# Performance work log

Measured on AMD Instinct MI355X. Metric: run time of the kernel, lower is better.

The kernel has to match this reference:

```python
import jax, jax.numpy as jnp
import numpy as np

K = 5  # filter_size (matches init_kwargs)


def _adaptive_pool_matrix(size: int, k: int) -> jnp.ndarray:
    """Row-stochastic [k, size] matrix replicating torch adaptive_avg_pool1d bins."""
    P = np.zeros((k, size), np.float32)
    for i in range(k):
        s = (i * size) // k
        e = -((-(i + 1) * size) // k)  # ceil((i+1)*size/k)
        P[i, s:e] = 1.0 / (e - s)
    return jnp.asarray(P)


def setup_inputs() -> dict:
    key = jax.random.key(0)
    k1, k2, k3 = jax.random.split(key, 3)
    B, Cin, Cout, H, W = 8, 32, 32, 256, 256
    x = jax.random.normal(k1, (B, Cin, H, W), jnp.float32)
    conv_w = jax.random.normal(k2, (Cout, Cin), jnp.float32) * (1.0 / np.sqrt(Cin))
    conv_b = jax.random.normal(k3, (Cout,), jnp.float32) * 0.01
    return {"x": x, "conv_w": conv_w, "conv_b": conv_b}


def reference(x, conv_w, conv_b):
    B, Cin, H, W = x.shape
    # 1x1 conv == channel-mixing einsum
    feat = jnp.einsum('bihw,oi->bohw', x, conv_w) + conv_b[None, :, None, None]
    C = feat.shape[1]
    # adaptive_avg_pool2d(feat, K) via static pooling matrices -> per-(b,c) KxK filter
    Ph = _adaptive_pool_matrix(H, K)
    Pw = _adaptive_pool_matrix(W, K)
    filt = jnp.einsum('kh,bchw,lw->bckl', Ph, feat, Pw)  # [B, C, K, K]
    # pad per original intent ('same' output), then grouped conv with groups=B*C
    pad = (K - 1) // 2
    if (K - 1) % 2 == 0:
        p = ((pad, pad), (pad, pad))
    else:
        p = ((pad + 1, pad), (pad + 1, pad))
    inp = feat.reshape(1, B * C, H, W)
    w = filt.reshape(B * C, 1, K, K)
    out = jax.lax.conv_general_dilated(
        inp, w, window_strides=(1, 1), padding=p,
        dimension_numbers=('NCHW', 'OIHW', 'NCHW'),
        feature_group_count=B * C)
    return out.reshape(B, C, H, W)
```

## Files before the change

kernel.cpp:

```cpp
#include <hip/hip_runtime.h>


#define CIN 32
#define COUT 32
#define HW 256
#define PLANE (HW * HW)
#define BATCH 8
#define KF 5
#define BIN 52

__global__ __launch_bounds__(256) void conv1x1_kernel(const float* __restrict__ x,
                                                      const float* __restrict__ Wm,
                                                      const float* __restrict__ bias,
                                                      float* __restrict__ feat) {
    int b  = blockIdx.x >> 6;
    int rg = blockIdx.x & 63;
    int p0 = rg * 1024 + threadIdx.x * 4;

    const float* xb = x + (size_t)b * CIN * PLANE + p0;
    float4 xv[CIN];
#pragma unroll
    for (int i = 0; i < CIN; ++i) xv[i] = *(const float4*)(xb + (size_t)i * PLANE);

    float* fb = feat + (size_t)b * COUT * PLANE + p0;
#pragma unroll 4
    for (int o = 0; o < COUT; ++o) {
        float bv = bias[o];
        float4 a; a.x = bv; a.y = bv; a.z = bv; a.w = bv;
#pragma unroll
        for (int i = 0; i < CIN; ++i) {
            float wv = Wm[o * CIN + i];
            a.x += wv * xv[i].x; a.y += wv * xv[i].y;
            a.z += wv * xv[i].z; a.w += wv * xv[i].w;
        }
        *(float4*)(fb + (size_t)o * PLANE) = a;
    }
}

__global__ __launch_bounds__(256) void pool_kernel(const float* __restrict__ feat,
                                                   float* __restrict__ filt) {
    int bo = blockIdx.x / KF;
    int k  = blockIdx.x % KF;
    int sk = (k * HW) / KF;
    int t  = threadIdx.x;
    int c4 = t & 63;
    int rq = t >> 6;

    const float* f = feat + (size_t)bo * PLANE + (sk + rq) * HW + c4 * 4;
    float4 a = {0.f, 0.f, 0.f, 0.f};
#pragma unroll
    for (int j = 0; j < 13; ++j) {
        float4 v = *(const float4*)(f + j * 4 * HW);
        a.x += v.x; a.y += v.y; a.z += v.z; a.w += v.w;
    }

    __shared__ float4 red[256];
    __shared__ float cols[256];
    red[t] = a;
    __syncthreads();
    if (t < 64) {
        float4 r0 = red[t], r1 = red[t + 64], r2 = red[t + 128], r3 = red[t + 192];
        cols[4 * t + 0] = r0.x + r1.x + r2.x + r3.x;
        cols[4 * t + 1] = r0.y + r1.y + r2.y + r3.y;
        cols[4 * t + 2] = r0.z + r1.z + r2.z + r3.z;
        cols[4 * t + 3] = r0.w + r1.w + r2.w + r3.w;
    }
    __syncthreads();
    if (t < KF) {
        int sl = (t * HW) / KF;
        float s = 0.f;
        for (int w = 0; w < BIN; ++w) s += cols[sl + w];
        filt[bo * 25 + k * KF + t] = s * (1.0f / (BIN * BIN));
    }
}

#define LROW 264
__global__ __launch_bounds__(256) void dwconv_kernel(const float* __restrict__ feat,
                                                     const float* __restrict__ filt,
                                                     float* __restrict__ out) {
    int bo    = blockIdx.y;
    int strip = blockIdx.x;
    int gy0   = strip * 32;
    int t     = threadIdx.x;

    __shared__ __align__(16) float s[36 * LROW];
    __shared__ float sfilt[25];
    if (t < 25) sfilt[t] = filt[bo * 25 + t];
    if (t < 144) {
        int lr = t >> 2, e = t & 3;
        int ci = (e < 2) ? (2 + e) : (258 + e);
        s[lr * LROW + ci] = 0.f;
    }

    const float* fb = feat + (size_t)bo * PLANE;
#pragma unroll
    for (int j = 0; j < 9; ++j) {
        int idx = t + 256 * j;
        int lr  = idx >> 6;
        int cx  = (idx & 63) * 4;
        int gy  = gy0 - 2 + lr;
        float4 v = {0.f, 0.f, 0.f, 0.f};
        if ((unsigned)gy < (unsigned)HW) v = *(const float4*)(fb + gy * HW + cx);
        *(float4*)(&s[lr * LROW + 4 + cx]) = v;
    }
    __syncthreads();

    float fw[25];
#pragma unroll
    for (int j = 0; j < 25; ++j) fw[j] = sfilt[j];

    int c = t;
    float w0[5], w1[5], w2[5], w3[5], w4[5];
#pragma unroll
    for (int j = 0; j < 5; ++j) {
        w0[j] = s[0 * LROW + 2 + c + j];
        w1[j] = s[1 * LROW + 2 + c + j];
        w2[j] = s[2 * LROW + 2 + c + j];
        w3[j] = s[3 * LROW + 2 + c + j];
    }
    float* ob = out + (size_t)bo * PLANE + (size_t)gy0 * HW + c;
#pragma unroll
    for (int r = 0; r < 32; ++r) {
#pragma unroll
        for (int j = 0; j < 5; ++j) w4[j] = s[(r + 4) * LROW + 2 + c + j];
        float acc = 0.f;
#pragma unroll
        for (int j = 0; j < 5; ++j) {
            acc += fw[0 * 5 + j] * w0[j];
            acc += fw[1 * 5 + j] * w1[j];
            acc += fw[2 * 5 + j] * w2[j];
            acc += fw[3 * 5 + j] * w3[j];
            acc += fw[4 * 5 + j] * w4[j];
        }
        ob[r * HW] = acc;
#pragma unroll
        for (int j = 0; j < 5; ++j) {
            w0[j] = w1[j]; w1[j] = w2[j]; w2[j] = w3[j]; w3[j] = w4[j];
        }
    }
}

extern "C" void kernel_launch(void* const* d_in, const int* in_sizes, int n_in,
                              void* d_out, int out_size, void* d_ws, size_t ws_size,
                              hipStream_t stream) {
    const float* x      = (const float*)d_in[0];
    const float* conv_w = (const float*)d_in[1];
    const float* conv_b = (const float*)d_in[2];
    float* out = (float*)d_out;

    float* feat = (float*)d_ws;
    float* filt = feat + (size_t)BATCH * COUT * PLANE;

    conv1x1_kernel<<<dim3(BATCH * 64), dim3(256), 0, stream>>>(x, conv_w, conv_b, feat);
    pool_kernel<<<dim3(BATCH * COUT * KF), dim3(256), 0, stream>>>(feat, filt);
    dwconv_kernel<<<dim3(8, BATCH * COUT), dim3(256), 0, stream>>>(feat, filt, out);
}
```

Before: 188.7 us.

## Fuse adaptive pooling into 1x1 conv via per-row partial sums and atomics

Merges the pooling pass into the 1x1 conv kernel. Each block now computes one full image row for all output channels, stages the conv output in LDS, sums each column bin and atomically adds into a zeroed filter buffer. The final division by the bin area moves into the depthwise conv kernel. This removes a full re-read of the feature map for pooling, at the cost of a memset, many atomics, a 32 KB LDS tile per block and a smaller per-thread workload.

Result: faster. 156.9 us (-16.8%).

```diff
diff --git a/kernel.cpp b/kernel.cpp
--- a/kernel.cpp
+++ b/kernel.cpp
@@ -9,74 +9,64 @@
 #define KF 5
 #define BIN 52
 
-__global__ __launch_bounds__(256) void conv1x1_kernel(const float* __restrict__ x,
-                                                      const float* __restrict__ Wm,
-                                                      const float* __restrict__ bias,
-                                                      float* __restrict__ feat) {
-    int b  = blockIdx.x >> 6;
-    int rg = blockIdx.x & 63;
-    int p0 = rg * 1024 + threadIdx.x * 4;
+__global__ __launch_bounds__(256) void conv1x1_pool_kernel(const float* __restrict__ x,
+                                                           const float* __restrict__ Wm,
+                                                           const float* __restrict__ bias,
+                                                           float* __restrict__ feat,
+                                                           float* __restrict__ filt_raw) {
+    int b   = blockIdx.x >> 8;
+    int row = blockIdx.x & 255;
+    int t   = threadIdx.x;
 
-    const float* xb = x + (size_t)b * CIN * PLANE + p0;
-    float4 xv[CIN];
+    __shared__ __align__(16) float lds[CIN * HW];
+
+    const float* xb = x + (size_t)b * CIN * PLANE + row * HW;
 #pragma unroll
-    for (int i = 0; i < CIN; ++i) xv[i] = *(const float4*)(xb + (size_t)i * PLANE);
+    for (int j = 0; j < 8; ++j) {
+        int idx = t + 256 * j;
+        int ch  = idx >> 6;
+        int c4  = (idx & 63) << 2;
+        *(float4*)&lds[ch * HW + c4] = *(const float4*)(xb + (size_t)ch * PLANE + c4);
+    }
+    __syncthreads();
 
-    float* fb = feat + (size_t)b * COUT * PLANE + p0;
-#pragma unroll 4
-    for (int o = 0; o < COUT; ++o) {
-        float bv = bias[o];
-        float4 a; a.x = bv; a.y = bv; a.z = bv; a.w = bv;
+    float acc[COUT];
 #pragma unroll
-        for (int i = 0; i < CIN; ++i) {
-            float wv = Wm[o * CIN + i];
-            a.x += wv * xv[i].x; a.y += wv * xv[i].y;
-            a.z += wv * xv[i].z; a.w += wv * xv[i].w;
-        }
-        *(float4*)(fb + (size_t)o * PLANE) = a;
-    }
-}
-
-__global__ __launch_bounds__(256) void pool_kernel(const float* __restrict__ feat,
-                                                   float* __restrict__ filt) {
-    int bo = blockIdx.x / KF;
-    int k  = blockIdx.x % KF;
-    int sk = (k * HW) / KF;
-    int t  = threadIdx.x;
-    int c4 = t & 63;
-    int rq = t >> 6;
-
-    const float* f = feat + (size_t)bo * PLANE + (sk + rq) * HW + c4 * 4;
-    float4 a = {0.f, 0.f, 0.f, 0.f};
+    for (int o = 0; o < COUT; ++o) acc[o] = bias[o];
 #pragma unroll
-    for (int j = 0; j < 13; ++j) {
-        float4 v = *(const float4*)(f + j * 4 * HW);
-        a.x += v.x; a.y += v.y; a.z += v.z; a.w += v.w;
+    for (int i = 0; i < CIN; ++i) {
+        float xi = lds[i * HW + t];
+#pragma unroll
+        for (int o = 0; o < COUT; ++o) acc[o] += Wm[o * CIN + i] * xi;
     }
 
-    __shared__ float4 red[256];
-    __shared__ float cols[256];
-    red[t] = a;
+    float* fb = feat + (size_t)b * COUT * PLANE + row * HW + t;
+#pragma unroll
+    for (int o = 0; o < COUT; ++o) fb[(size_t)o * PLANE] = acc[o];
+
     __syncthreads();
-    if (t < 64) {
-        float4 r0 = red[t], r1 = red[t + 64], r2 = red[t + 128], r3 = red[t + 192];
-        cols[4 * t + 0] = r0.x + r1.x + r2.x + r3.x;
-        cols[4 * t + 1] = r0.y + r1.y + r2.y + r3.y;
-        cols[4 * t + 2] = r0.z + r1.z + r2.z + r3.z;
-        cols[4 * t + 3] = r0.w + r1.w + r2.w + r3.w;
-    }
+#pragma unroll
+    for (int o = 0; o < COUT; ++o) lds[o * HW + t] = acc[o];
     __syncthreads();
-    if (t < KF) {
-        int sl = (t * HW) / KF;
+
+    if (t < COUT * KF) {
+        int o  = t / KF;
+        int l  = t - o * KF;
+        int sl = (l * HW) / KF;
         float s = 0.f;
-        for (int w = 0; w < BIN; ++w) s += cols[sl + w];
-        filt[bo * 25 + k * KF + t] = s * (1.0f / (BIN * BIN));
+        for (int w = 0; w < BIN; ++w) s += lds[o * HW + sl + w];
+        float* dst = filt_raw + (size_t)(b * COUT + o) * 25 + l;
+#pragma unroll
+        for (int k = 0; k < KF; ++k) {
+            int sk = (k * HW) / KF;
+            if (row >= sk && row < sk + BIN) atomicAdd(dst + k * KF, s);
+        }
     }
 }
 
 #define LROW 264
 __global__ __launch_bounds__(256) void dwconv_kernel(const float* __restrict__ feat,
-                                                     const float* __restrict__ filt,
+                                                     const float* __restrict__ filt_raw,
                                                      float* __restrict__ out) {
     int bo    = blockIdx.y;
     int strip = blockIdx.x;
@@ -85,7 +75,7 @@
 
     __shared__ __align__(16) float s[36 * LROW];
     __shared__ float sfilt[25];
-    if (t < 25) sfilt[t] = filt[bo * 25 + t];
+    if (t < 25) sfilt[t] = filt_raw[bo * 25 + t] * (1.0f / (52.0f * 52.0f));
     if (t < 144) {
         int lr = t >> 2, e = t & 3;
         int ci = (e < 2) ? (2 + e) : (258 + e);
@@ -151,7 +141,7 @@
     float* feat = (float*)d_ws;
     float* filt = feat + (size_t)BATCH * COUT * PLANE;
 
-    conv1x1_kernel<<<dim3(BATCH * 64), dim3(256), 0, stream>>>(x, conv_w, conv_b, feat);
-    pool_kernel<<<dim3(BATCH * COUT * KF), dim3(256), 0, stream>>>(feat, filt);
+    hipMemsetAsync(filt, 0, BATCH * COUT * 25 * sizeof(float), stream);
+    conv1x1_pool_kernel<<<dim3(BATCH * 256), dim3(256), 0, stream>>>(x, conv_w, conv_b, feat, filt);
     dwconv_kernel<<<dim3(8, BATCH * COUT), dim3(256), 0, stream>>>(feat, filt, out);
 }
```
